# Kernel optimization log

Hardware: AMD Instinct MI355X
Metric: run time of the kernel (lower is better)

## Reference

```python
import jax, jax.numpy as jnp
import numpy as np
import math

B, T, E, F, K, NUM_CONV, H = 32, 2048, 512, 512, 7, 4, 8
EPS = 1e-5


def _ln2(x):
    # fresh nn.LayerNorm(x.size()[1:]): normalize jointly over last two dims, weight=1 bias=0
    mu = jnp.mean(x, axis=(-2, -1), keepdims=True)
    var = jnp.var(x, axis=(-2, -1), keepdims=True)
    return (x - mu) * jax.lax.rsqrt(var + EPS)


def _ds_conv(x, dw_w, dw_b, pw_w, pw_b):
    # x: (B, C, T); depthwise conv (groups=C) then pointwise 1x1
    C = x.shape[1]
    k = dw_w.shape[-1]
    y = jax.lax.conv_general_dilated(
        x, dw_w, window_strides=(1,), padding=[(k // 2, k // 2)],
        dimension_numbers=('NCH', 'OIH', 'NCH'), feature_group_count=C)
    y = y + dw_b[None, :, None]
    y = jnp.einsum('oc,bct->bot', pw_w, y) + pw_b[None, :, None]
    return y


def _pos_enc(n, e):
    # pe[i, 0::2] = sin(i * div), pe[i, 1::2] = cos(i * div); returns (n, 1, e)
    pos = jnp.arange(n, dtype=jnp.float32)[:, None]
    div = jnp.exp(jnp.arange(0, e, 2, dtype=jnp.float32) * (-math.log(10000.0) / e))
    pe = jnp.zeros((n, e), dtype=jnp.float32)
    pe = pe.at[:, 0::2].set(jnp.sin(pos * div)).at[:, 1::2].set(jnp.cos(pos * div))
    return pe[:, None, :]


def setup_inputs() -> dict:
    key = jax.random.key(0)
    ks = jax.random.split(key, 20)
    w = lambda i, shape: (jax.random.normal(ks[i], shape, jnp.float32) * 0.02)
    return {
        'x': jax.random.normal(ks[0], (B, T, E), jnp.float32),
        'dw1_w': w(1, (E, 1, K)), 'dw1_b': w(2, (E,)),
        'pw1_w': w(3, (F, E)), 'pw1_b': w(4, (F,)),
        'dw2_w': w(5, (F, 1, K)), 'dw2_b': w(6, (F,)),
        'pw2_w': w(7, (F, F)), 'pw2_b': w(8, (F,)),
        'wq': w(9, (F, F)), 'bq': w(10, (F,)),
        'wk': w(11, (F, F)), 'bk': w(12, (F,)),
        'wv': w(13, (F, F)), 'bv': w(14, (F,)),
        'wp': w(15, (F, F)), 'bp': w(16, (F,)),
        'ff_w': w(17, (F, F)), 'ff_b': w(18, (F,)),
    }


def reference(x, dw1_w, dw1_b, pw1_w, pw1_b, dw2_w, dw2_b, pw2_w, pw2_b,
              wq, bq, wk, bk, wv, bv, wp, bp, ff_w, ff_b):
    b, t, e = x.shape
    # positional encoding: pe[:x.size(0)] -> (B,1,E), broadcast over T (faithful quirk)
    x = x + _pos_enc(b, e)
    x = jnp.transpose(x, (0, 2, 1))          # (B, E, T)
    x = _ln2(x)
    x = _ds_conv(x, dw1_w, dw1_b, pw1_w, pw1_b)   # (B, F, T)
    for _ in range(NUM_CONV - 1):                 # shared conv weights each iter (faithful)
        x = x + _ds_conv(_ln2(x), dw2_w, dw2_b, pw2_w, pw2_b)
    # attention: code permutes to (T, B, F) so attention attends across the batch axis
    y = jnp.transpose(_ln2(x), (2, 0, 1))    # (T, B, F)
    x = jnp.transpose(x, (2, 0, 1))          # (T, B, F)
    f = x.shape[-1]
    hd = f // H
    q = (y @ wq.T + bq).reshape(t, b, H, hd).transpose(0, 2, 1, 3)  # (T, H, B, hd)
    k = (y @ wk.T + bk).reshape(t, b, H, hd).transpose(0, 2, 1, 3)
    v = (y @ wv.T + bv).reshape(t, b, H, hd).transpose(0, 2, 1, 3)
    att = jnp.einsum('thbd,thcd->thbc', q, k) * (1.0 / math.sqrt(hd))
    att = jax.nn.softmax(att, axis=-1)
    yo = jnp.einsum('thbc,thcd->thbd', att, v)
    yo = yo.transpose(0, 2, 1, 3).reshape(t, b, f)
    yo = yo @ wp.T + bp
    x = x + yo
    y = _ln2(x)                               # norm over last-two dims (B, F)
    y = y @ ff_w.T + ff_b
    x = x + y
    return jnp.transpose(x, (1, 0, 2))        # (B, T, F)
```

## Files before the change

kernel.cpp:

```cpp
#include <hip/hip_runtime.h>
#include <math.h>

constexpr int B_ = 32, T_ = 2048, E_ = 512, F_ = 512, KW = 7, H_ = 8;
constexpr float EPS_ = 1e-5f;

typedef unsigned short bfu;
typedef __attribute__((ext_vector_type(8))) unsigned short ushort8v;
typedef __attribute__((ext_vector_type(8))) short short8v;
typedef __attribute__((ext_vector_type(4))) short short4v;
typedef __attribute__((ext_vector_type(4))) float f32x4;
typedef __attribute__((ext_vector_type(16))) float f32x16;
typedef const __attribute__((address_space(1))) void* gp1_t;
typedef __attribute__((address_space(3))) void* lp3_t;

__device__ __forceinline__ float b2f(bfu u) {
    return __uint_as_float(((unsigned)u) << 16);
}
__device__ __forceinline__ bfu f2b(float f) {
    unsigned i = __float_as_uint(f);
    i += 0x7fffu + ((i >> 16) & 1u);
    return (bfu)(i >> 16);
}

template <typename T> __device__ __forceinline__ void st4(T* p, size_t i, float a, float b, float c, float d);
template <> __device__ __forceinline__ void st4<bfu>(bfu* p, size_t i, float a, float b, float c, float d) {
    ushort4 u = { f2b(a), f2b(b), f2b(c), f2b(d) };
    *(ushort4*)(p + i) = u;
}
template <> __device__ __forceinline__ void st4<float>(float* p, size_t i, float a, float b, float c, float d) {
    float4 u = { a, b, c, d };
    *(float4*)(p + i) = u;
}

__global__ void zero_kernel(float* p, int n) {
    int i = blockIdx.x * 256 + threadIdx.x;
    if (i < n) p[i] = 0.f;
}

__global__ __launch_bounds__(256) void prep(const float* __restrict__ w0, const float* __restrict__ w1,
                                            const float* __restrict__ w2, const float* __restrict__ w3,
                                            const float* __restrict__ w4, const float* __restrict__ w5,
                                            const float* __restrict__ w6,
                                            bfu* __restrict__ wb, float* __restrict__ pe) {
    int idx = blockIdx.x * 256 + threadIdx.x;
    if (idx < 7 * 65536) {
        int w = idx >> 16, off = (idx & 65535) * 4;
        const float* src = w0;
        switch (w) {
            case 1: src = w1; break; case 2: src = w2; break; case 3: src = w3; break;
            case 4: src = w4; break; case 5: src = w5; break; case 6: src = w6; break;
            default: break;
        }
        float4 v = *(const float4*)(src + off);
        ushort4 u = { f2b(v.x), f2b(v.y), f2b(v.z), f2b(v.w) };
        *(ushort4*)(wb + (size_t)w * 262144 + off) = u;
    } else {
        int i = (idx - 7 * 65536) * 4;
        if (i < 16384) {
            #pragma unroll
            for (int e4 = 0; e4 < 4; e4++) {
                int ii = i + e4;
                int b = ii >> 9, e = ii & 511;
                float div = expf(-(float)(e & ~1) * (logf(10000.0f) / (float)E_));
                float ang = (float)b * div;
                pe[ii] = (e & 1) ? cosf(ang) : sinf(ang);
            }
        }
    }
}

__global__ __launch_bounds__(256) void add_pe(const float* __restrict__ x,
                                              const float* __restrict__ pe,
                                              bfu* __restrict__ out,
                                              float* __restrict__ stats) {
    size_t base = (size_t)blockIdx.x * 4096;
    int b = (int)(base >> 20);
    float sum = 0.f, sq = 0.f;
    #pragma unroll
    for (int u = 0; u < 4; u++) {
        size_t i = base + u * 1024 + threadIdx.x * 4;
        int e = (int)(i & 511);
        float4 xv = *(const float4*)(x + i);
        float4 pv = *(const float4*)(pe + (b << 9) + e);
        float a0 = xv.x + pv.x, a1 = xv.y + pv.y, a2 = xv.z + pv.z, a3 = xv.w + pv.w;
        ushort4 o = { f2b(a0), f2b(a1), f2b(a2), f2b(a3) };
        *(ushort4*)(out + i) = o;
        sum += a0 + a1 + a2 + a3;
        sq  += a0 * a0 + a1 * a1 + a2 * a2 + a3 * a3;
    }
    #pragma unroll
    for (int off = 32; off > 0; off >>= 1) {
        sum += __shfl_down(sum, off, 64);
        sq  += __shfl_down(sq,  off, 64);
    }
    __shared__ float ss[8];
    int lane = threadIdx.x & 63, wv = threadIdx.x >> 6;
    if (lane == 0) { ss[wv] = sum; ss[4 + wv] = sq; }
    __syncthreads();
    if (threadIdx.x == 0) {
        atomicAdd(&stats[2 * b],     ss[0] + ss[1] + ss[2] + ss[3]);
        atomicAdd(&stats[2 * b + 1], ss[4] + ss[5] + ss[6] + ss[7]);
    }
}

__device__ __forceinline__ float ln_rstd(float sumsq, float mu, float invL) {
    float var = fmaxf(sumsq * invL - mu * mu, 0.f);
    return rsqrtf(var + EPS_);
}

__global__ __launch_bounds__(256) void dwconv_nhwc(const bfu* __restrict__ x,
                                                   const float* __restrict__ stats,
                                                   const float* __restrict__ w,
                                                   const float* __restrict__ bias,
                                                   bfu* __restrict__ out) {
    __shared__ float ws[64 * 57];
    int tid = threadIdx.x;
    int b = blockIdx.z;
    for (int i = tid; i < F_ * KW; i += 256) {
        int f = i / KW, dt = i - f * KW;
        ws[(f >> 3) * 57 + (f & 7) * 7 + dt] = w[i];
    }
    __syncthreads();
    const float invL = 1.0f / (float)(F_ * T_);
    float mu   = stats[2 * b] * invL;
    float rstd = ln_rstd(stats[2 * b + 1], mu, invL);
    int f0 = (tid & 63) * 8;
    int t  = blockIdx.x * 4 + (tid >> 6);
    const bfu* xb = x + (size_t)b * T_ * F_;
    const float* wc_ = &ws[(tid & 63) * 57];
    float acc[8];
    #pragma unroll
    for (int j = 0; j < 8; j++) acc[j] = bias[f0 + j];
    #pragma unroll
    for (int dt = 0; dt < KW; dt++) {
        int tt = t + dt - KW / 2;
        if (tt >= 0 && tt < T_) {
            ushort8v v = *(const ushort8v*)(xb + (size_t)tt * F_ + f0);
            #pragma unroll
            for (int j = 0; j < 8; j++)
                acc[j] += wc_[j * 7 + dt] * ((b2f(v[j]) - mu) * rstd);
        }
    }
    ushort8v o;
    #pragma unroll
    for (int j = 0; j < 8; j++) o[j] = f2b(acc[j]);
    *(ushort8v*)(out + ((size_t)b * T_ + t) * F_ + f0) = o;
}

template <typename OutT, int GMODE, int NMAT>
__global__ __launch_bounds__(256, 4) void gemm_mfma(const bfu* __restrict__ A,
                                                    const bfu* __restrict__ Wb,
                                                    const float* __restrict__ bias0,
                                                    const float* __restrict__ bias1,
                                                    const float* __restrict__ bias2,
                                                    const bfu* res,
                                                    OutT* out0, OutT* out1, OutT* out2,
                                                    int out_transpose, float* stats) {
    constexpr int Kd = 512;
    constexpr int NWG = 2048 * NMAT;
    __shared__ bfu As[2][4096];
    __shared__ bfu Bs[2][4096];
    int id  = blockIdx.x;
    int swz = (id & 7) * (NWG >> 3) + (id >> 3);
    int mt  = swz % (4 * NMAT);
    int r0  = (swz / (4 * NMAT)) * 128;
    int mat = mt >> 2;
    int m0  = (mt & 3) * 128;
    int tid  = threadIdx.x;
    int wave = tid >> 6, lane = tid & 63;
    int wr = (wave >> 1) * 64, wc = (wave & 1) * 64;
    int lg = lane >> 4,  lr = lane & 15;

    const char* Ab = (const char*)A  + (size_t)r0 * 1024;
    const char* Bb = (const char*)Wb + (size_t)mt * 128 * 1024;
    int rS = (wave << 4) + (lane >> 2);
    int kb = (lane & 3) << 4;
    int ldsoff = wave << 10;

    f32x4 acc[4][4];
    #pragma unroll
    for (int ni = 0; ni < 4; ni++)
        #pragma unroll
        for (int mi = 0; mi < 4; mi++)
            acc[ni][mi] = (f32x4){0.f, 0.f, 0.f, 0.f};

    #define STAGE(p, k0)                                                                   \
        do {                                                                               \
            size_t koff_ = (size_t)((k0) << 1);                                            \
            const char* a0_ = Ab + (size_t)rS * 1024 + koff_ + kb;                         \
            const char* b0_ = Bb + (size_t)rS * 1024 + koff_ + kb;                         \
            char* ad_ = (char*)As + (p) * 8192 + ldsoff;                                   \
            char* bd_ = (char*)Bs + (p) * 8192 + ldsoff;                                   \
            __builtin_amdgcn_global_load_lds((gp1_t)a0_,           (lp3_t)ad_,          16, 0, 0); \
            __builtin_amdgcn_global_load_lds((gp1_t)(a0_ + 65536), (lp3_t)(ad_ + 4096), 16, 0, 0); \
            __builtin_amdgcn_global_load_lds((gp1_t)b0_,           (lp3_t)bd_,          16, 0, 0); \
            __builtin_amdgcn_global_load_lds((gp1_t)(b0_ + 65536), (lp3_t)(bd_ + 4096), 16, 0, 0); \
        } while (0)

    STAGE(0, 0);
    #pragma unroll 2
    for (int it = 0; it < 16; ++it) {
        int cur = it & 1;
        if (it < 15) {
            STAGE(cur ^ 1, (it + 1) * 32);
            asm volatile("s_waitcnt vmcnt(4)" ::: "memory");
        } else {
            asm volatile("s_waitcnt vmcnt(0)" ::: "memory");
        }
        __builtin_amdgcn_sched_barrier(0);
        __builtin_amdgcn_s_barrier();
        __builtin_amdgcn_sched_barrier(0);
        const bfu* Ap = &As[cur][(wr + lr) * 32 + lg * 8];
        const bfu* Bp = &Bs[cur][(wc + lr) * 32 + lg * 8];
        short8v a[4], bb[4];
        #pragma unroll
        for (int mi = 0; mi < 4; mi++) a[mi]  = *(const short8v*)(Ap + mi * 512);
        #pragma unroll
        for (int ni = 0; ni < 4; ni++) bb[ni] = *(const short8v*)(Bp + ni * 512);
        #pragma unroll
        for (int ni = 0; ni < 4; ni++)
            #pragma unroll
            for (int mi = 0; mi < 4; mi++)
                acc[ni][mi] = __builtin_amdgcn_mfma_f32_16x16x32_bf16(bb[ni], a[mi], acc[ni][mi], 0, 0, 0);
        asm volatile("s_waitcnt lgkmcnt(0)" ::: "memory");
        __builtin_amdgcn_sched_barrier(0);
        __builtin_amdgcn_s_barrier();
    }
    #undef STAGE

    const float* bias = (NMAT == 1 || mat == 0) ? bias0 : (mat == 1 ? bias1 : bias2);
    OutT*        outb = (NMAT == 1 || mat == 0) ? out0  : (mat == 1 ? out1  : out2);

    float sAcc0 = 0.f, sAcc1 = 0.f, qAcc0 = 0.f, qAcc1 = 0.f;
    #pragma unroll
    for (int mi = 0; mi < 4; mi++) {
        int r = r0 + wr + mi * 16 + lr;
        #pragma unroll
        for (int ni = 0; ni < 4; ni++) {
            int mo = m0 + wc + ni * 16 + lg * 4;
            float4 bv = *(const float4*)(bias + mo);
            float v0 = acc[ni][mi][0] + bv.x;
            float v1 = acc[ni][mi][1] + bv.y;
            float v2 = acc[ni][mi][2] + bv.z;
            float v3 = acc[ni][mi][3] + bv.w;
            if (res) {
                ushort4 rv = *(const ushort4*)(res + (size_t)r * 512 + mo);
                v0 += b2f(rv.x); v1 += b2f(rv.y); v2 += b2f(rv.z); v3 += b2f(rv.w);
            }
            if (GMODE) {
                float s = v0 + v1 + v2 + v3;
                float q = v0 * v0 + v1 * v1 + v2 * v2 + v3 * v3;
                if (mi < 2) { sAcc0 += s; qAcc0 += q; }
                else        { sAcc1 += s; qAcc1 += q; }
            }
            if (!out_transpose) {
                st4(outb, (size_t)r * 512 + mo, v0, v1, v2, v3);
            } else {
                int t = r >> 5, bb2 = r & 31;
                st4(outb, ((size_t)bb2 * T_ + t) * 512 + mo, v0, v1, v2, v3);
            }
        }
    }
    if (GMODE == 1) {
        float s = sAcc0 + sAcc1, q = qAcc0 + qAcc1;
        #pragma unroll
        for (int off = 32; off > 0; off >>= 1) {
            s += __shfl_down(s, off, 64);
            q += __shfl_down(q, off, 64);
        }
        if (lane == 0) {
            int g = r0 >> 11;
            atomicAdd(&stats[2 * g], s);
            atomicAdd(&stats[2 * g + 1], q);
        }
    } else if (GMODE == 2) {
        #pragma unroll
        for (int off = 32; off > 0; off >>= 1) {
            sAcc0 += __shfl_down(sAcc0, off, 64); qAcc0 += __shfl_down(qAcc0, off, 64);
            sAcc1 += __shfl_down(sAcc1, off, 64); qAcc1 += __shfl_down(qAcc1, off, 64);
        }
        if (lane == 0) {
            int g0 = (r0 >> 5) + (wr >> 5);
            atomicAdd(&stats[2 * g0],     sAcc0);
            atomicAdd(&stats[2 * g0 + 1], qAcc0);
            atomicAdd(&stats[2 * g0 + 2], sAcc1);
            atomicAdd(&stats[2 * g0 + 3], qAcc1);
        }
    }
}

__global__ __launch_bounds__(256) void bt2tb_ln(const bfu* __restrict__ x,
                                                const float* __restrict__ stats,
                                                bfu* __restrict__ xa,
                                                bfu* __restrict__ yln) {
    size_t i = ((size_t)blockIdx.x * 256 + threadIdx.x) * 8;
    int f = (int)(i & 511);
    size_t bt = i >> 9;
    int t = (int)(bt & 2047);
    int b = (int)(bt >> 11);
    const float invL = 1.0f / (float)(F_ * T_);
    float mu   = stats[2 * b] * invL;
    float rstd = ln_rstd(stats[2 * b + 1], mu, invL);
    ushort8v v = *(const ushort8v*)(x + i);
    size_t dst = (((size_t)t * B_ + b) << 9) + f;
    *(ushort8v*)(xa + dst) = v;
    ushort8v o;
    #pragma unroll
    for (int j = 0; j < 8; j++) o[j] = f2b((b2f(v[j]) - mu) * rstd);
    *(ushort8v*)(yln + dst) = o;
}

__global__ __launch_bounds__(256) void ln_apply(const bfu* __restrict__ x,
                                                const float* __restrict__ stats,
                                                bfu* __restrict__ out,
                                                float invL, int shift) {
    size_t i = ((size_t)blockIdx.x * 256 + threadIdx.x) * 8;
    int g = (int)(i >> shift);
    float mu   = stats[2 * g] * invL;
    float rstd = ln_rstd(stats[2 * g + 1], mu, invL);
    ushort8v v = *(const ushort8v*)(x + i);
    ushort8v o;
    #pragma unroll
    for (int j = 0; j < 8; j++) o[j] = f2b((b2f(v[j]) - mu) * rstd);
    *(ushort8v*)(out + i) = o;
}

__global__ __launch_bounds__(256) void attention_mfma(const bfu* __restrict__ Q,
                                                      const bfu* __restrict__ K,
                                                      const bfu* __restrict__ V,
                                                      bfu* __restrict__ O) {
    __shared__ bfu vt[4][64 * 36];
    int tid = threadIdx.x;
    int wave = tid >> 6, lane = tid & 63;
    int wid = blockIdx.x * 4 + wave;
    int t = wid >> 3, h = wid & 7;
    int lh = lane >> 5, lm = lane & 31;
    size_t base = (size_t)t * (B_ * F_) + (size_t)h * 64;

    short8v qf[4], kf[4];
    const bfu* qrow = Q + base + (size_t)lm * F_ + lh * 8;
    const bfu* krow = K + base + (size_t)lm * F_ + lh * 8;
    #pragma unroll
    for (int s = 0; s < 4; s++) {
        qf[s] = *(const short8v*)(qrow + s * 16);
        kf[s] = *(const short8v*)(krow + s * 16);
    }
    bfu* vt_w = vt[wave];
    {
        int c = lane >> 1, d0 = (lane & 1) * 32;
        const bfu* vrow = V + base + (size_t)c * F_ + d0;
        #pragma unroll
        for (int j = 0; j < 4; j++) {
            ushort8v vv = *(const ushort8v*)(vrow + j * 8);
            #pragma unroll
            for (int e = 0; e < 8; e++)
                vt_w[(d0 + j * 8 + e) * 36 + c] = vv[e];
        }
    }
    f32x16 st;
    #pragma unroll
    for (int r = 0; r < 16; r++) st[r] = 0.f;
    #pragma unroll
    for (int s = 0; s < 4; s++)
        st = __builtin_amdgcn_mfma_f32_32x32x16_bf16(kf[s], qf[s], st, 0, 0, 0);

    float p[16];
    float mx = -1e30f;
    #pragma unroll
    for (int r = 0; r < 16; r++) { p[r] = st[r] * 0.125f; mx = fmaxf(mx, p[r]); }
    mx = fmaxf(mx, __shfl_xor(mx, 32, 64));
    float sum = 0.f;
    #pragma unroll
    for (int r = 0; r < 16; r++) { p[r] = expf(p[r] - mx); sum += p[r]; }
    sum += __shfl_xor(sum, 32, 64);
    float inv = 1.0f / sum;
    short8v pa[2];
    #pragma unroll
    for (int j = 0; j < 8; j++) {
        pa[0][j] = (short)f2b(p[j] * inv);
        pa[1][j] = (short)f2b(p[8 + j] * inv);
    }
    f32x16 oacc[2];
    #pragma unroll
    for (int dt = 0; dt < 2; dt++)
        #pragma unroll
        for (int r = 0; r < 16; r++) oacc[dt][r] = 0.f;
    #pragma unroll
    for (int dt = 0; dt < 2; dt++) {
        const bfu* vr = vt_w + (dt * 32 + lm) * 36 + lh * 4;
        #pragma unroll
        for (int kh = 0; kh < 2; kh++) {
            short4v b0 = *(const short4v*)(vr + kh * 16);
            short4v b1 = *(const short4v*)(vr + kh * 16 + 8);
            short8v bf;
            #pragma unroll
            for (int e = 0; e < 4; e++) { bf[e] = b0[e]; bf[4 + e] = b1[e]; }
            oacc[dt] = __builtin_amdgcn_mfma_f32_32x32x16_bf16(pa[kh], bf, oacc[dt], 0, 0, 0);
        }
    }
    bfu* orow = O + base + lm;
    #pragma unroll
    for (int dt = 0; dt < 2; dt++)
        #pragma unroll
        for (int r = 0; r < 16; r++) {
            int b = (r & 3) + 8 * (r >> 2) + 4 * lh;
            orow[(size_t)b * F_ + dt * 32] = f2b(oacc[dt][r]);
        }
}

extern "C" void kernel_launch(void* const* d_in, const int* in_sizes, int n_in,
                              void* d_out, int out_size, void* d_ws, size_t ws_size,
                              hipStream_t stream) {
    const float* x     = (const float*)d_in[0];
    const float* dw1_w = (const float*)d_in[1];
    const float* dw1_b = (const float*)d_in[2];
    const float* pw1_w = (const float*)d_in[3];
    const float* pw1_b = (const float*)d_in[4];
    const float* dw2_w = (const float*)d_in[5];
    const float* dw2_b = (const float*)d_in[6];
    const float* pw2_w = (const float*)d_in[7];
    const float* pw2_b = (const float*)d_in[8];
    const float* wq = (const float*)d_in[9];   const float* bq = (const float*)d_in[10];
    const float* wk = (const float*)d_in[11];  const float* bk = (const float*)d_in[12];
    const float* wv = (const float*)d_in[13];  const float* bv = (const float*)d_in[14];
    const float* wp = (const float*)d_in[15];  const float* bp = (const float*)d_in[16];
    const float* ffw = (const float*)d_in[17]; const float* ffb = (const float*)d_in[18];
    float* out = (float*)d_out;

    const size_t SZ = (size_t)B_ * F_ * T_;
    const size_t WN = (size_t)F_ * F_;

    float* stats = (float*)d_ws;
    float* stA = stats;
    float* st1 = stats + 128;
    float* st2 = stats + 256;
    float* st3 = stats + 384;
    float* st4 = stats + 512;
    float* stT = stats + 1024;
    float* peTab = stats + 8192;
    bfu*   wBuf  = (bfu*)(peTab + 16384);
    bfu* wb_pw1 = wBuf + 0 * WN;
    bfu* wb_pw2 = wBuf + 1 * WN;
    bfu* wb_q   = wBuf + 2 * WN;
    bfu* wb_p   = wBuf + 5 * WN;
    bfu* wb_ff  = wBuf + 6 * WN;
    bfu* bufX = (bfu*)d_ws + (1 << 21);
    bfu* bufC = bufX + SZ;
    bfu* bufY = bufC + SZ;
    bfu* bufK = bufY + SZ;
    bfu* bufV = bufK + SZ;

    zero_kernel<<<32, 256, 0, stream>>>(stats, 8192);
    prep<<<1808, 256, 0, stream>>>(pw1_w, pw2_w, wq, wk, wv, wp, ffw, wBuf, peTab);
    add_pe<<<8192, 256, 0, stream>>>(x, peTab, bufX, stA);

    dwconv_nhwc<<<dim3(T_ / 4, 1, B_), 256, 0, stream>>>(bufX, stA, dw1_w, dw1_b, bufC);
    gemm_mfma<bfu, 1, 1><<<2048, 256, 0, stream>>>(bufC, wb_pw1, pw1_b, pw1_b, pw1_b,
                                                   nullptr, bufX, bufX, bufX, 0, st1);

    float* sts[3] = { st2, st3, st4 };
    for (int it = 0; it < 3; ++it) {
        float* sin_ = (it == 0) ? st1 : sts[it - 1];
        dwconv_nhwc<<<dim3(T_ / 4, 1, B_), 256, 0, stream>>>(bufX, sin_, dw2_w, dw2_b, bufC);
        gemm_mfma<bfu, 1, 1><<<2048, 256, 0, stream>>>(bufC, wb_pw2, pw2_b, pw2_b, pw2_b,
                                                       bufX, bufX, bufX, bufX, 0, sts[it]);
    }

    bt2tb_ln<<<16384, 256, 0, stream>>>(bufX, st4, bufC, bufY);

    gemm_mfma<bfu, 0, 3><<<6144, 256, 0, stream>>>(bufY, wb_q, bq, bk, bv,
                                                   nullptr, bufX, bufK, bufV, 0, nullptr);

    attention_mfma<<<4096, 256, 0, stream>>>(bufX, bufK, bufV, bufY);

    gemm_mfma<bfu, 2, 1><<<2048, 256, 0, stream>>>(bufY, wb_p, bp, bp, bp,
                                                   bufC, bufK, bufK, bufK, 0, stT);

    ln_apply<<<16384, 256, 0, stream>>>(bufK, stT, bufX, 1.0f / (float)(B_ * F_), 14);

    gemm_mfma<float, 0, 1><<<2048, 256, 0, stream>>>(bufX, wb_ff, ffb, ffb, ffb,
                                                     bufK, out, out, out, 1, nullptr);
}
```

Measured before the change: 1.600 ms.

## Retile GEMM to 128x256 with 8 waves, triple-buffered swizzled LDS and BK=64

Rebuilds the shared MFMA GEMM kernel around 512-thread blocks that each compute a 128x256 output tile with a 64-wide K step. It adds a three-stage global_load_lds pipeline, an XOR-swizzled LDS layout to avoid bank conflicts, split fragment loads that overlap with MFMA issue, and s_setprio around the MFMA blocks. The aim is more operand reuse per LDS byte and better hiding of global memory latency. In exchange it uses 144 KB of LDS and allows only one block per CU, so occupancy drops.

Measured after the change: 1.613 ms. No clear change (+0.8%).

```diff
diff --git a/kernel.cpp b/kernel.cpp
--- a/kernel.cpp
+++ b/kernel.cpp
@@ -148,7 +148,7 @@
 }
 
 template <typename OutT, int GMODE, int NMAT>
-__global__ __launch_bounds__(256, 4) void gemm_mfma(const bfu* __restrict__ A,
+__global__ __launch_bounds__(512, 1) void gemm_mfma(const bfu* __restrict__ A,
                                                     const bfu* __restrict__ Wb,
                                                     const float* __restrict__ bias0,
                                                     const float* __restrict__ bias1,
@@ -156,75 +156,97 @@
                                                     const bfu* res,
                                                     OutT* out0, OutT* out1, OutT* out2,
                                                     int out_transpose, float* stats) {
-    constexpr int Kd = 512;
-    constexpr int NWG = 2048 * NMAT;
-    __shared__ bfu As[2][4096];
-    __shared__ bfu Bs[2][4096];
+    constexpr int NWG = 1024 * NMAT;
+    __shared__ bfu smem[3 * 24576];
     int id  = blockIdx.x;
     int swz = (id & 7) * (NWG >> 3) + (id >> 3);
-    int mt  = swz % (4 * NMAT);
-    int r0  = (swz / (4 * NMAT)) * 128;
-    int mat = mt >> 2;
-    int m0  = (mt & 3) * 128;
-    int tid  = threadIdx.x;
-    int wave = tid >> 6, lane = tid & 63;
-    int wr = (wave >> 1) * 64, wc = (wave & 1) * 64;
-    int lg = lane >> 4,  lr = lane & 15;
-
-    const char* Ab = (const char*)A  + (size_t)r0 * 1024;
-    const char* Bb = (const char*)Wb + (size_t)mt * 128 * 1024;
-    int rS = (wave << 4) + (lane >> 2);
-    int kb = (lane & 3) << 4;
-    int ldsoff = wave << 10;
+    int mt  = swz % (2 * NMAT);
+    int r0  = (swz / (2 * NMAT)) * 128;
+    int mat = mt >> 1;
+    int m0  = (mt & 1) * 256;
+    int tid = threadIdx.x;
+    int w = tid >> 6, l = tid & 63;
+    int wm = w >> 2, wn = w & 3;
+    int lr = l & 15, lg = l >> 4, e = lr & 7;
+
+    int srow   = (w << 3) + (l >> 3);
+    int schunk = (l & 7) ^ ((l >> 3) & 7);
+    size_t sOff = (size_t)srow * 512 + (size_t)schunk * 8;
+    int wbyte = w << 10;
+    const bfu* Apan = A  + (size_t)r0 * 512;
+    const bfu* Bpan = Wb + (size_t)mt * 256 * 512;
 
     f32x4 acc[4][4];
     #pragma unroll
-    for (int ni = 0; ni < 4; ni++)
+    for (int nj = 0; nj < 4; nj++)
         #pragma unroll
         for (int mi = 0; mi < 4; mi++)
-            acc[ni][mi] = (f32x4){0.f, 0.f, 0.f, 0.f};
-
-    #define STAGE(p, k0)                                                                   \
-        do {                                                                               \
-            size_t koff_ = (size_t)((k0) << 1);                                            \
-            const char* a0_ = Ab + (size_t)rS * 1024 + koff_ + kb;                         \
-            const char* b0_ = Bb + (size_t)rS * 1024 + koff_ + kb;                         \
-            char* ad_ = (char*)As + (p) * 8192 + ldsoff;                                   \
-            char* bd_ = (char*)Bs + (p) * 8192 + ldsoff;                                   \
-            __builtin_amdgcn_global_load_lds((gp1_t)a0_,           (lp3_t)ad_,          16, 0, 0); \
-            __builtin_amdgcn_global_load_lds((gp1_t)(a0_ + 65536), (lp3_t)(ad_ + 4096), 16, 0, 0); \
-            __builtin_amdgcn_global_load_lds((gp1_t)b0_,           (lp3_t)bd_,          16, 0, 0); \
-            __builtin_amdgcn_global_load_lds((gp1_t)(b0_ + 65536), (lp3_t)(bd_ + 4096), 16, 0, 0); \
+            acc[nj][mi] = (f32x4){0.f, 0.f, 0.f, 0.f};
+
+    #define STAGE(kt, bb)                                                                        \
+        do {                                                                                     \
+            const bfu* Ag_ = Apan + (size_t)(kt) * 64 + sOff;                                    \
+            const bfu* Bg_ = Bpan + (size_t)(kt) * 64 + sOff;                                    \
+            char* Ad_ = (char*)smem + (bb) * 49152 + wbyte;                                      \
+            char* Bd_ = (char*)smem + (bb) * 49152 + 16384 + wbyte;                              \
+            __builtin_amdgcn_global_load_lds((gp1_t)Ag_,              (lp3_t)Ad_,           16, 0, 0); \
+            __builtin_amdgcn_global_load_lds((gp1_t)(Ag_ +  64*512),  (lp3_t)(Ad_ +  8192), 16, 0, 0); \
+            __builtin_amdgcn_global_load_lds((gp1_t)Bg_,              (lp3_t)Bd_,           16, 0, 0); \
+            __builtin_amdgcn_global_load_lds((gp1_t)(Bg_ +  64*512),  (lp3_t)(Bd_ +  8192), 16, 0, 0); \
+            __builtin_amdgcn_global_load_lds((gp1_t)(Bg_ + 128*512),  (lp3_t)(Bd_ + 16384), 16, 0, 0); \
+            __builtin_amdgcn_global_load_lds((gp1_t)(Bg_ + 192*512),  (lp3_t)(Bd_ + 24576), 16, 0, 0); \
         } while (0)
 
     STAGE(0, 0);
-    #pragma unroll 2
-    for (int it = 0; it < 16; ++it) {
-        int cur = it & 1;
-        if (it < 15) {
-            STAGE(cur ^ 1, (it + 1) * 32);
-            asm volatile("s_waitcnt vmcnt(4)" ::: "memory");
-        } else {
-            asm volatile("s_waitcnt vmcnt(0)" ::: "memory");
-        }
+    STAGE(1, 1);
+    STAGE(2, 2);
+
+    int aR = wm * 64 + lr, bR = wn * 64 + lr;
+    int c0 = ((lg) ^ e) * 8;
+    int c1 = ((4 | lg) ^ e) * 8;
+
+    #pragma unroll
+    for (int it = 0; it < 8; ++it) {
+        int cur = it % 3;
+        if (it < 6)       asm volatile("s_waitcnt vmcnt(12)" ::: "memory");
+        else if (it == 6) asm volatile("s_waitcnt vmcnt(6)"  ::: "memory");
+        else              asm volatile("s_waitcnt vmcnt(0)"  ::: "memory");
         __builtin_amdgcn_sched_barrier(0);
         __builtin_amdgcn_s_barrier();
         __builtin_amdgcn_sched_barrier(0);
-        const bfu* Ap = &As[cur][(wr + lr) * 32 + lg * 8];
-        const bfu* Bp = &Bs[cur][(wc + lr) * 32 + lg * 8];
-        short8v a[4], bb[4];
-        #pragma unroll
-        for (int mi = 0; mi < 4; mi++) a[mi]  = *(const short8v*)(Ap + mi * 512);
-        #pragma unroll
-        for (int ni = 0; ni < 4; ni++) bb[ni] = *(const short8v*)(Bp + ni * 512);
-        #pragma unroll
-        for (int ni = 0; ni < 4; ni++)
+        const bfu* bufA = smem + cur * 24576;
+        const bfu* bufB = bufA + 8192;
+        short8v aF0[4], bF0[4], aF1[4], bF1[4];
+        #pragma unroll
+        for (int mi = 0; mi < 4; mi++) aF0[mi] = *(const short8v*)(bufA + (aR + mi * 16) * 64 + c0);
+        #pragma unroll
+        for (int nj = 0; nj < 4; nj++) bF0[nj] = *(const short8v*)(bufB + (bR + nj * 16) * 64 + c0);
+        __builtin_amdgcn_sched_barrier(0);
+        #pragma unroll
+        for (int mi = 0; mi < 4; mi++) aF1[mi] = *(const short8v*)(bufA + (aR + mi * 16) * 64 + c1);
+        #pragma unroll
+        for (int nj = 0; nj < 4; nj++) bF1[nj] = *(const short8v*)(bufB + (bR + nj * 16) * 64 + c1);
+        __builtin_amdgcn_sched_barrier(0);
+        asm volatile("s_waitcnt lgkmcnt(8)" ::: "memory");
+        __builtin_amdgcn_sched_barrier(0);
+        __builtin_amdgcn_s_setprio(1);
+        #pragma unroll
+        for (int nj = 0; nj < 4; nj++)
             #pragma unroll
             for (int mi = 0; mi < 4; mi++)
-                acc[ni][mi] = __builtin_amdgcn_mfma_f32_16x16x32_bf16(bb[ni], a[mi], acc[ni][mi], 0, 0, 0);
+                acc[nj][mi] = __builtin_amdgcn_mfma_f32_16x16x32_bf16(bF0[nj], aF0[mi], acc[nj][mi], 0, 0, 0);
         asm volatile("s_waitcnt lgkmcnt(0)" ::: "memory");
         __builtin_amdgcn_sched_barrier(0);
+        #pragma unroll
+        for (int nj = 0; nj < 4; nj++)
+            #pragma unroll
+            for (int mi = 0; mi < 4; mi++)
+                acc[nj][mi] = __builtin_amdgcn_mfma_f32_16x16x32_bf16(bF1[nj], aF1[mi], acc[nj][mi], 0, 0, 0);
+        __builtin_amdgcn_s_setprio(0);
+        __builtin_amdgcn_sched_barrier(0);
         __builtin_amdgcn_s_barrier();
+        __builtin_amdgcn_sched_barrier(0);
+        if (it + 3 < 8) STAGE(it + 3, (it + 3) % 3);
     }
     #undef STAGE
 
@@ -234,15 +256,15 @@
     float sAcc0 = 0.f, sAcc1 = 0.f, qAcc0 = 0.f, qAcc1 = 0.f;
     #pragma unroll
     for (int mi = 0; mi < 4; mi++) {
-        int r = r0 + wr + mi * 16 + lr;
-        #pragma unroll
-        for (int ni = 0; ni < 4; ni++) {
-            int mo = m0 + wc + ni * 16 + lg * 4;
+        int r = r0 + wm * 64 + mi * 16 + lr;
+        #pragma unroll
+        for (int nj = 0; nj < 4; nj++) {
+            int mo = m0 + wn * 64 + nj * 16 + lg * 4;
             float4 bv = *(const float4*)(bias + mo);
-            float v0 = acc[ni][mi][0] + bv.x;
-            float v1 = acc[ni][mi][1] + bv.y;
-            float v2 = acc[ni][mi][2] + bv.z;
-            float v3 = acc[ni][mi][3] + bv.w;
+            float v0 = acc[nj][mi][0] + bv.x;
+            float v1 = acc[nj][mi][1] + bv.y;
+            float v2 = acc[nj][mi][2] + bv.z;
+            float v3 = acc[nj][mi][3] + bv.w;
             if (res) {
                 ushort4 rv = *(const ushort4*)(res + (size_t)r * 512 + mo);
                 v0 += b2f(rv.x); v1 += b2f(rv.y); v2 += b2f(rv.z); v3 += b2f(rv.w);
@@ -268,7 +290,7 @@
             s += __shfl_down(s, off, 64);
             q += __shfl_down(q, off, 64);
         }
-        if (lane == 0) {
+        if (l == 0) {
             int g = r0 >> 11;
             atomicAdd(&stats[2 * g], s);
             atomicAdd(&stats[2 * g + 1], q);
@@ -279,8 +301,8 @@
             sAcc0 += __shfl_down(sAcc0, off, 64); qAcc0 += __shfl_down(qAcc0, off, 64);
             sAcc1 += __shfl_down(sAcc1, off, 64); qAcc1 += __shfl_down(qAcc1, off, 64);
         }
-        if (lane == 0) {
-            int g0 = (r0 >> 5) + (wr >> 5);
+        if (l == 0) {
+            int g0 = (r0 >> 5) + wm * 2;
             atomicAdd(&stats[2 * g0],     sAcc0);
             atomicAdd(&stats[2 * g0 + 1], qAcc0);
             atomicAdd(&stats[2 * g0 + 2], sAcc1);
@@ -455,29 +477,29 @@
     add_pe<<<8192, 256, 0, stream>>>(x, peTab, bufX, stA);
 
     dwconv_nhwc<<<dim3(T_ / 4, 1, B_), 256, 0, stream>>>(bufX, stA, dw1_w, dw1_b, bufC);
-    gemm_mfma<bfu, 1, 1><<<2048, 256, 0, stream>>>(bufC, wb_pw1, pw1_b, pw1_b, pw1_b,
+    gemm_mfma<bfu, 1, 1><<<1024, 512, 0, stream>>>(bufC, wb_pw1, pw1_b, pw1_b, pw1_b,
                                                    nullptr, bufX, bufX, bufX, 0, st1);
 
     float* sts[3] = { st2, st3, st4 };
     for (int it = 0; it < 3; ++it) {
         float* sin_ = (it == 0) ? st1 : sts[it - 1];
         dwconv_nhwc<<<dim3(T_ / 4, 1, B_), 256, 0, stream>>>(bufX, sin_, dw2_w, dw2_b, bufC);
-        gemm_mfma<bfu, 1, 1><<<2048, 256, 0, stream>>>(bufC, wb_pw2, pw2_b, pw2_b, pw2_b,
+        gemm_mfma<bfu, 1, 1><<<1024, 512, 0, stream>>>(bufC, wb_pw2, pw2_b, pw2_b, pw2_b,
                                                        bufX, bufX, bufX, bufX, 0, sts[it]);
     }
 
     bt2tb_ln<<<16384, 256, 0, stream>>>(bufX, st4, bufC, bufY);
 
-    gemm_mfma<bfu, 0, 3><<<6144, 256, 0, stream>>>(bufY, wb_q, bq, bk, bv,
+    gemm_mfma<bfu, 0, 3><<<3072, 512, 0, stream>>>(bufY, wb_q, bq, bk, bv,
                                                    nullptr, bufX, bufK, bufV, 0, nullptr);
 
     attention_mfma<<<4096, 256, 0, stream>>>(bufX, bufK, bufV, bufY);
 
-    gemm_mfma<bfu, 2, 1><<<2048, 256, 0, stream>>>(bufY, wb_p, bp, bp, bp,
+    gemm_mfma<bfu, 2, 1><<<1024, 512, 0, stream>>>(bufY, wb_p, bp, bp, bp,
                                                    bufC, bufK, bufK, bufK, 0, stT);
 
     ln_apply<<<16384, 256, 0, stream>>>(bufK, stT, bufX, 1.0f / (float)(B_ * F_), 14);
 
-    gemm_mfma<float, 0, 1><<<2048, 256, 0, stream>>>(bufX, wb_ff, ffb, ffb, ffb,
+    gemm_mfma<float, 0, 1><<<1024, 512, 0, stream>>>(bufX, wb_ff, ffb, ffb, ffb,
                                                      bufK, out, out, out, 1, nullptr);
 }
```

## Make GEMM persistent with triple-buffered LDS pipeline and swizzled layout

Applied to the files above, without the earlier changes.

Turns the MFMA GEMM into a persistent kernel: 768 workgroups each walk a contiguous range of 128x128 tiles. K-slices are prefetched across tile boundaries through a three-stage LDS ring, so loads for the next tile overlap the current tile's tail and epilogue. LDS columns are XOR-swizzled to reduce bank conflicts, and MFMA sections get raised wave priority. Occupancy drops to 3 blocks/SM, and the more complex vmcnt accounting makes the tail pipeline fragile.

Result: no change. 1.627 ms (+1.7%).

```diff
diff --git a/kernel.cpp b/kernel.cpp
--- a/kernel.cpp
+++ b/kernel.cpp
@@ -148,7 +148,7 @@
 }
 
 template <typename OutT, int GMODE, int NMAT>
-__global__ __launch_bounds__(256, 4) void gemm_mfma(const bfu* __restrict__ A,
+__global__ __launch_bounds__(256, 3) void gemm_mfma(const bfu* __restrict__ A,
                                                     const bfu* __restrict__ Wb,
                                                     const float* __restrict__ bias0,
                                                     const float* __restrict__ bias1,
@@ -156,26 +156,36 @@
                                                     const bfu* res,
                                                     OutT* out0, OutT* out1, OutT* out2,
                                                     int out_transpose, float* stats) {
-    constexpr int Kd = 512;
-    constexpr int NWG = 2048 * NMAT;
-    __shared__ bfu As[2][4096];
-    __shared__ bfu Bs[2][4096];
-    int id  = blockIdx.x;
-    int swz = (id & 7) * (NWG >> 3) + (id >> 3);
-    int mt  = swz % (4 * NMAT);
-    int r0  = (swz / (4 * NMAT)) * 128;
-    int mat = mt >> 2;
-    int m0  = (mt & 3) * 128;
-    int tid  = threadIdx.x;
-    int wave = tid >> 6, lane = tid & 63;
-    int wr = (wave >> 1) * 64, wc = (wave & 1) * 64;
-    int lg = lane >> 4,  lr = lane & 15;
-
-    const char* Ab = (const char*)A  + (size_t)r0 * 1024;
-    const char* Bb = (const char*)Wb + (size_t)mt * 128 * 1024;
-    int rS = (wave << 4) + (lane >> 2);
-    int kb = (lane & 3) << 4;
-    int ldsoff = wave << 10;
+    constexpr int NMT = 4 * NMAT;
+    constexpr int NT  = 512 * NMT;
+    constexpr int NWG = 768;
+    __shared__ bfu smem[24576];
+
+    int v = ((blockIdx.x & 7) * (NWG >> 3)) + (blockIdx.x >> 3);
+    constexpr int q = NT / NWG, rem = NT % NWG;
+    int start = v * q + (v < rem ? v : rem);
+    int cnt   = q + (v < rem ? 1 : 0);
+
+    int tid = threadIdx.x;
+    int w = tid >> 6, l = tid & 63;
+    int wr = (w >> 1) * 64, wc = (w & 1) * 64;
+    int lr = l & 15, lg = l >> 4;
+    int ca = (lg ^ (lr & 3)) * 8;
+
+    int sr = (w << 4) + (l >> 2);
+    int sc = l & 3;
+    int laneOff = sr * 1024 + (((sc ^ (sr & 3))) << 4);
+
+    #define STAGE(aB_, bB_, ks_, bi_)                                                              \
+        do {                                                                                        \
+            const char* ag_ = (aB_) + (ks_) * 64 + laneOff;                                         \
+            const char* bg_ = (bB_) + (ks_) * 64 + laneOff;                                         \
+            char* d_ = (char*)smem + (bi_) * 16384 + (w << 10);                                     \
+            __builtin_amdgcn_global_load_lds((gp1_t)ag_,           (lp3_t)d_,            16, 0, 0); \
+            __builtin_amdgcn_global_load_lds((gp1_t)(ag_ + 65536), (lp3_t)(d_ + 4096),   16, 0, 0); \
+            __builtin_amdgcn_global_load_lds((gp1_t)bg_,           (lp3_t)(d_ + 8192),   16, 0, 0); \
+            __builtin_amdgcn_global_load_lds((gp1_t)(bg_ + 65536), (lp3_t)(d_ + 12288),  16, 0, 0); \
+        } while (0)
 
     f32x4 acc[4][4];
     #pragma unroll
@@ -184,109 +194,126 @@
         for (int mi = 0; mi < 4; mi++)
             acc[ni][mi] = (f32x4){0.f, 0.f, 0.f, 0.f};
 
-    #define STAGE(p, k0)                                                                   \
-        do {                                                                               \
-            size_t koff_ = (size_t)((k0) << 1);                                            \
-            const char* a0_ = Ab + (size_t)rS * 1024 + koff_ + kb;                         \
-            const char* b0_ = Bb + (size_t)rS * 1024 + koff_ + kb;                         \
-            char* ad_ = (char*)As + (p) * 8192 + ldsoff;                                   \
-            char* bd_ = (char*)Bs + (p) * 8192 + ldsoff;                                   \
-            __builtin_amdgcn_global_load_lds((gp1_t)a0_,           (lp3_t)ad_,          16, 0, 0); \
-            __builtin_amdgcn_global_load_lds((gp1_t)(a0_ + 65536), (lp3_t)(ad_ + 4096), 16, 0, 0); \
-            __builtin_amdgcn_global_load_lds((gp1_t)b0_,           (lp3_t)bd_,          16, 0, 0); \
-            __builtin_amdgcn_global_load_lds((gp1_t)(b0_ + 65536), (lp3_t)(bd_ + 4096), 16, 0, 0); \
-        } while (0)
-
-    STAGE(0, 0);
-    #pragma unroll 2
-    for (int it = 0; it < 16; ++it) {
-        int cur = it & 1;
-        if (it < 15) {
-            STAGE(cur ^ 1, (it + 1) * 32);
-            asm volatile("s_waitcnt vmcnt(4)" ::: "memory");
-        } else {
-            asm volatile("s_waitcnt vmcnt(0)" ::: "memory");
-        }
-        __builtin_amdgcn_sched_barrier(0);
-        __builtin_amdgcn_s_barrier();
-        __builtin_amdgcn_sched_barrier(0);
-        const bfu* Ap = &As[cur][(wr + lr) * 32 + lg * 8];
-        const bfu* Bp = &Bs[cur][(wc + lr) * 32 + lg * 8];
-        short8v a[4], bb[4];
-        #pragma unroll
-        for (int mi = 0; mi < 4; mi++) a[mi]  = *(const short8v*)(Ap + mi * 512);
-        #pragma unroll
-        for (int ni = 0; ni < 4; ni++) bb[ni] = *(const short8v*)(Bp + ni * 512);
+    int tl = start;
+    int mt = tl % NMT;
+    int r0 = (tl / NMT) << 7;
+    const char* aB = (const char*)A  + (size_t)r0 * 1024;
+    const char* bB = (const char*)Wb + (size_t)mt * 131072;
+
+    STAGE(aB, bB, 0, 0);
+    STAGE(aB, bB, 1, 1);
+    int bof = 0;
+
+    for (int tix = 0; tix < cnt; ++tix) {
+        bool last = (tix == cnt - 1);
+        int nmt = mt, nr0 = r0;
+        const char *naB = aB, *nbB = bB;
+        if (!last) {
+            nmt = (mt + 1 == NMT) ? 0 : mt + 1;
+            nr0 = (nmt == 0) ? r0 + 128 : r0;
+            naB = (const char*)A  + (size_t)nr0 * 1024;
+            nbB = (const char*)Wb + (size_t)nmt * 131072;
+        }
+        #pragma unroll
+        for (int ks = 0; ks < 16; ++ks) {
+            int cb = (bof + ks) % 3;
+            int sb = (bof + ks + 2) % 3;
+            if (ks < 14)      STAGE(aB, bB, ks + 2, sb);
+            else if (!last)   STAGE(naB, nbB, ks - 14, sb);
+            if (!last || ks < 14) asm volatile("s_waitcnt vmcnt(8)" ::: "memory");
+            else if (ks == 14)    asm volatile("s_waitcnt vmcnt(4)" ::: "memory");
+            else                  asm volatile("s_waitcnt vmcnt(0)" ::: "memory");
+            __builtin_amdgcn_s_barrier();
+            const bfu* bufA = smem + cb * 8192;
+            const bfu* bufB = bufA + 4096;
+            short8v a[4], bb[4];
+            #pragma unroll
+            for (int mi = 0; mi < 4; mi++)
+                a[mi]  = *(const short8v*)(bufA + (wr + mi * 16 + lr) * 32 + ca);
+            #pragma unroll
+            for (int ni = 0; ni < 4; ni++)
+                bb[ni] = *(const short8v*)(bufB + (wc + ni * 16 + lr) * 32 + ca);
+            __builtin_amdgcn_s_setprio(1);
+            #pragma unroll
+            for (int ni = 0; ni < 4; ni++)
+                #pragma unroll
+                for (int mi = 0; mi < 4; mi++)
+                    acc[ni][mi] = __builtin_amdgcn_mfma_f32_16x16x32_bf16(bb[ni], a[mi], acc[ni][mi], 0, 0, 0);
+            __builtin_amdgcn_s_setprio(0);
+            __builtin_amdgcn_s_barrier();
+        }
+
+        {
+            int mat = mt >> 2;
+            int m0  = (mt & 3) * 128;
+            const float* bias = (NMAT == 1 || mat == 0) ? bias0 : (mat == 1 ? bias1 : bias2);
+            OutT*        outb = (NMAT == 1 || mat == 0) ? out0  : (mat == 1 ? out1  : out2);
+            float sAcc0 = 0.f, sAcc1 = 0.f, qAcc0 = 0.f, qAcc1 = 0.f;
+            #pragma unroll
+            for (int mi = 0; mi < 4; mi++) {
+                int r = r0 + wr + mi * 16 + lr;
+                #pragma unroll
+                for (int ni = 0; ni < 4; ni++) {
+                    int mo = m0 + wc + ni * 16 + lg * 4;
+                    float4 bv = *(const float4*)(bias + mo);
+                    float v0 = acc[ni][mi][0] + bv.x;
+                    float v1 = acc[ni][mi][1] + bv.y;
+                    float v2 = acc[ni][mi][2] + bv.z;
+                    float v3 = acc[ni][mi][3] + bv.w;
+                    if (res) {
+                        ushort4 rv = *(const ushort4*)(res + (size_t)r * 512 + mo);
+                        v0 += b2f(rv.x); v1 += b2f(rv.y); v2 += b2f(rv.z); v3 += b2f(rv.w);
+                    }
+                    if (GMODE) {
+                        float s = v0 + v1 + v2 + v3;
+                        float qq = v0 * v0 + v1 * v1 + v2 * v2 + v3 * v3;
+                        if (mi < 2) { sAcc0 += s; qAcc0 += qq; }
+                        else        { sAcc1 += s; qAcc1 += qq; }
+                    }
+                    if (!out_transpose) {
+                        st4(outb, (size_t)r * 512 + mo, v0, v1, v2, v3);
+                    } else {
+                        int t = r >> 5, bb2 = r & 31;
+                        st4(outb, ((size_t)bb2 * T_ + t) * 512 + mo, v0, v1, v2, v3);
+                    }
+                }
+            }
+            if (GMODE == 1) {
+                float s = sAcc0 + sAcc1, qq = qAcc0 + qAcc1;
+                #pragma unroll
+                for (int off = 32; off > 0; off >>= 1) {
+                    s  += __shfl_down(s,  off, 64);
+                    qq += __shfl_down(qq, off, 64);
+                }
+                if (l == 0) {
+                    int g = r0 >> 11;
+                    atomicAdd(&stats[2 * g], s);
+                    atomicAdd(&stats[2 * g + 1], qq);
+                }
+            } else if (GMODE == 2) {
+                #pragma unroll
+                for (int off = 32; off > 0; off >>= 1) {
+                    sAcc0 += __shfl_down(sAcc0, off, 64); qAcc0 += __shfl_down(qAcc0, off, 64);
+                    sAcc1 += __shfl_down(sAcc1, off, 64); qAcc1 += __shfl_down(qAcc1, off, 64);
+                }
+                if (l == 0) {
+                    int g0 = (r0 >> 5) + (wr >> 5);
+                    atomicAdd(&stats[2 * g0],     sAcc0);
+                    atomicAdd(&stats[2 * g0 + 1], qAcc0);
+                    atomicAdd(&stats[2 * g0 + 2], sAcc1);
+                    atomicAdd(&stats[2 * g0 + 3], qAcc1);
+                }
+            }
+        }
         #pragma unroll
         for (int ni = 0; ni < 4; ni++)
             #pragma unroll
             for (int mi = 0; mi < 4; mi++)
-                acc[ni][mi] = __builtin_amdgcn_mfma_f32_16x16x32_bf16(bb[ni], a[mi], acc[ni][mi], 0, 0, 0);
-        asm volatile("s_waitcnt lgkmcnt(0)" ::: "memory");
-        __builtin_amdgcn_sched_barrier(0);
-        __builtin_amdgcn_s_barrier();
+                acc[ni][mi] = (f32x4){0.f, 0.f, 0.f, 0.f};
+        bof = (bof + 1) % 3;
+        mt = nmt; r0 = nr0; aB = naB; bB = nbB;
     }
     #undef STAGE
-
-    const float* bias = (NMAT == 1 || mat == 0) ? bias0 : (mat == 1 ? bias1 : bias2);
-    OutT*        outb = (NMAT == 1 || mat == 0) ? out0  : (mat == 1 ? out1  : out2);
-
-    float sAcc0 = 0.f, sAcc1 = 0.f, qAcc0 = 0.f, qAcc1 = 0.f;
-    #pragma unroll
-    for (int mi = 0; mi < 4; mi++) {
-        int r = r0 + wr + mi * 16 + lr;
-        #pragma unroll
-        for (int ni = 0; ni < 4; ni++) {
-            int mo = m0 + wc + ni * 16 + lg * 4;
-            float4 bv = *(const float4*)(bias + mo);
-            float v0 = acc[ni][mi][0] + bv.x;
-            float v1 = acc[ni][mi][1] + bv.y;
-            float v2 = acc[ni][mi][2] + bv.z;
-            float v3 = acc[ni][mi][3] + bv.w;
-            if (res) {
-                ushort4 rv = *(const ushort4*)(res + (size_t)r * 512 + mo);
-                v0 += b2f(rv.x); v1 += b2f(rv.y); v2 += b2f(rv.z); v3 += b2f(rv.w);
-            }
-            if (GMODE) {
-                float s = v0 + v1 + v2 + v3;
-                float q = v0 * v0 + v1 * v1 + v2 * v2 + v3 * v3;
-                if (mi < 2) { sAcc0 += s; qAcc0 += q; }
-                else        { sAcc1 += s; qAcc1 += q; }
-            }
-            if (!out_transpose) {
-                st4(outb, (size_t)r * 512 + mo, v0, v1, v2, v3);
-            } else {
-                int t = r >> 5, bb2 = r & 31;
-                st4(outb, ((size_t)bb2 * T_ + t) * 512 + mo, v0, v1, v2, v3);
-            }
-        }
-    }
-    if (GMODE == 1) {
-        float s = sAcc0 + sAcc1, q = qAcc0 + qAcc1;
-        #pragma unroll
-        for (int off = 32; off > 0; off >>= 1) {
-            s += __shfl_down(s, off, 64);
-            q += __shfl_down(q, off, 64);
-        }
-        if (lane == 0) {
-            int g = r0 >> 11;
-            atomicAdd(&stats[2 * g], s);
-            atomicAdd(&stats[2 * g + 1], q);
-        }
-    } else if (GMODE == 2) {
-        #pragma unroll
-        for (int off = 32; off > 0; off >>= 1) {
-            sAcc0 += __shfl_down(sAcc0, off, 64); qAcc0 += __shfl_down(qAcc0, off, 64);
-            sAcc1 += __shfl_down(sAcc1, off, 64); qAcc1 += __shfl_down(qAcc1, off, 64);
-        }
-        if (lane == 0) {
-            int g0 = (r0 >> 5) + (wr >> 5);
-            atomicAdd(&stats[2 * g0],     sAcc0);
-            atomicAdd(&stats[2 * g0 + 1], qAcc0);
-            atomicAdd(&stats[2 * g0 + 2], sAcc1);
-            atomicAdd(&stats[2 * g0 + 3], qAcc1);
-        }
-    }
 }
 
 __global__ __launch_bounds__(256) void bt2tb_ln(const bfu* __restrict__ x,
@@ -455,29 +482,29 @@
     add_pe<<<8192, 256, 0, stream>>>(x, peTab, bufX, stA);
 
     dwconv_nhwc<<<dim3(T_ / 4, 1, B_), 256, 0, stream>>>(bufX, stA, dw1_w, dw1_b, bufC);
-    gemm_mfma<bfu, 1, 1><<<2048, 256, 0, stream>>>(bufC, wb_pw1, pw1_b, pw1_b, pw1_b,
-                                                   nullptr, bufX, bufX, bufX, 0, st1);
+    gemm_mfma<bfu, 1, 1><<<768, 256, 0, stream>>>(bufC, wb_pw1, pw1_b, pw1_b, pw1_b,
+                                                  nullptr, bufX, bufX, bufX, 0, st1);
 
     float* sts[3] = { st2, st3, st4 };
     for (int it = 0; it < 3; ++it) {
         float* sin_ = (it == 0) ? st1 : sts[it - 1];
         dwconv_nhwc<<<dim3(T_ / 4, 1, B_), 256, 0, stream>>>(bufX, sin_, dw2_w, dw2_b, bufC);
-        gemm_mfma<bfu, 1, 1><<<2048, 256, 0, stream>>>(bufC, wb_pw2, pw2_b, pw2_b, pw2_b,
-                                                       bufX, bufX, bufX, bufX, 0, sts[it]);
+        gemm_mfma<bfu, 1, 1><<<768, 256, 0, stream>>>(bufC, wb_pw2, pw2_b, pw2_b, pw2_b,
+                                                      bufX, bufX, bufX, bufX, 0, sts[it]);
     }
 
     bt2tb_ln<<<16384, 256, 0, stream>>>(bufX, st4, bufC, bufY);
 
-    gemm_mfma<bfu, 0, 3><<<6144, 256, 0, stream>>>(bufY, wb_q, bq, bk, bv,
-                                                   nullptr, bufX, bufK, bufV, 0, nullptr);
+    gemm_mfma<bfu, 0, 3><<<768, 256, 0, stream>>>(bufY, wb_q, bq, bk, bv,
+                                                  nullptr, bufX, bufK, bufV, 0, nullptr);
 
     attention_mfma<<<4096, 256, 0, stream>>>(bufX, bufK, bufV, bufY);
 
-    gemm_mfma<bfu, 2, 1><<<2048, 256, 0, stream>>>(bufY, wb_p, bp, bp, bp,
-                                                   bufC, bufK, bufK, bufK, 0, stT);
+    gemm_mfma<bfu, 2, 1><<<768, 256, 0, stream>>>(bufY, wb_p, bp, bp, bp,
+                                                  bufC, bufK, bufK, bufK, 0, stT);
 
     ln_apply<<<16384, 256, 0, stream>>>(bufK, stT, bufX, 1.0f / (float)(B_ * F_), 14);
 
-    gemm_mfma<float, 0, 1><<<2048, 256, 0, stream>>>(bufX, wb_ff, ffb, ffb, ffb,
-                                                     bufK, out, out, out, 1, nullptr);
-}
+    gemm_mfma<float, 0, 1><<<768, 256, 0, stream>>>(bufX, wb_ff, ffb, ffb, ffb,
+                                                    bufK, out, out, out, 1, nullptr);
+}
```
